# Kernel optimization log

Hardware: AMD Instinct MI355X
Metric: run time of the kernel (lower is better)

Reference implementation:

```python
import jax, jax.numpy as jnp
import numpy as np

NUM_HEADS = 16
INACTIVE = 4          # cfg_comp.attention_heads_inactive
SIG_DIM = 64          # cfg_comp.attention_heads_signature_dim
MLP_HIDDEN = 512      # cfg_comp.attention_heads_inference_mlp_hidden


def setup_inputs() -> dict:
    key = jax.random.key(0)
    ks = jax.random.split(key, 16)
    S, B, E = 2048, 2, 1024
    def xavier(k, shape, gain=1.0):
        fan_in, fan_out = shape[1], shape[0]
        a = gain * np.sqrt(6.0 / (fan_in + fan_out))
        return jax.random.uniform(k, shape, jnp.float32, -a, a)
    g = 1.0 / np.sqrt(2.0)
    return {
        "query": jax.random.normal(ks[0], (S, B, E), jnp.float32),
        "q_w": xavier(ks[1], (E, E), g), "q_b": jnp.zeros((E,), jnp.float32),
        "k_w": xavier(ks[2], (E, E), g), "k_b": jnp.zeros((E,), jnp.float32),
        "v_w": xavier(ks[3], (E, E), g), "v_b": jnp.zeros((E,), jnp.float32),
        "out_w": xavier(ks[4], (E, E)), "out_b": jnp.zeros((E,), jnp.float32),
        "inf1_w": xavier(ks[5], (MLP_HIDDEN, E), np.sqrt(2.0)),
        "inf1_b": jnp.zeros((MLP_HIDDEN,), jnp.float32),
        "inf2_w": xavier(ks[6], (SIG_DIM, MLP_HIDDEN), np.sqrt(2.0)),
        "inf2_b": jnp.zeros((SIG_DIM,), jnp.float32),
        "head_sig": jax.random.normal(ks[7], (NUM_HEADS, SIG_DIM), jnp.float32)
                    * np.sqrt(2.0 / (NUM_HEADS + SIG_DIM)),
    }


def _head_mask(query, inf1_w, inf1_b, inf2_w, inf2_b, head_sig):
    # inference_masking_step: (S, B, E) -> binary mask (B, H, S)
    t = jax.nn.relu(query @ inf1_w.T + inf1_b)          # (S, B, hidden)
    t = t @ inf2_w.T + inf2_b                            # (S, B, sig)
    s = t @ head_sig.T                                   # (S, B, H) head scores
    keep = NUM_HEADS - INACTIVE
    kth = jax.lax.top_k(s, keep)[0][..., -1]             # (S, B) kth-largest score
    mask = (s >= kth[..., None]).astype(query.dtype)     # 1 at top-`keep` heads
    mask = jax.lax.stop_gradient(mask)                   # scatter of constants in torch
    return jnp.transpose(mask, (1, 2, 0))                # (B, H, S)


def reference(query, q_w, q_b, k_w, k_b, v_w, v_b, out_w, out_b,
              inf1_w, inf1_b, inf2_w, inf2_b, head_sig):
    S, B, E = query.shape
    H, D = NUM_HEADS, E // NUM_HEADS
    scaling = D ** (-0.5)

    q = (query @ q_w.T + q_b) * scaling                  # (S, B, E)
    k = query @ k_w.T + k_b
    v = query @ v_w.T + v_b
    # (S, B, E) -> (B, H, S, D)
    to_bhsd = lambda x: jnp.transpose(x.reshape(S, B, H, D), (1, 2, 0, 3))
    q, k, v = to_bhsd(q), to_bhsd(k), to_bhsd(v)

    attn = jax.nn.softmax(jnp.einsum("bhqd,bhkd->bhqk", q, k), axis=-1)
    o = jnp.einsum("bhqk,bhkd->bhqd", attn, v)           # (B, H, S, D)

    mask = _head_mask(query, inf1_w, inf1_b, inf2_w, inf2_b, head_sig)  # (B, H, S)
    o = o * mask[..., None]                              # gate per head per position

    out = jnp.transpose(o, (2, 0, 1, 3)).reshape(S, B, E)
    return out @ out_w.T + out_b
```

## Files before the change

kernel.cpp:

```cpp
#include <hip/hip_runtime.h>
#include <hip/hip_bf16.h>

#define S_LEN 2048
#define BATCH 2
#define EDIM 1024
#define NHEAD 16
#define DHEAD 64
#define HIDDEN 512
#define SIGD 64
#define KEEP 12

typedef __attribute__((ext_vector_type(8))) short bf16x8;
typedef __attribute__((ext_vector_type(4))) float f32x4;

static __device__ __forceinline__ float bf2f(short s) {
  unsigned int u = ((unsigned int)(unsigned short)s) << 16;
  float f; __builtin_memcpy(&f, &u, 4); return f;
}
static __device__ __forceinline__ short f2bf(float f) {
  unsigned int u; __builtin_memcpy(&u, &f, 4);
  u += 0x7fffu + ((u >> 16) & 1u);
  return (short)(u >> 16);
}

#if __has_builtin(__builtin_amdgcn_exp2f)
static __device__ __forceinline__ float fexp2(float x) { return __builtin_amdgcn_exp2f(x); }
#else
static __device__ __forceinline__ float fexp2(float x) { return exp2f(x); }
#endif

static __device__ __forceinline__ void gl_lds16(const short* g, short* l) {
  __builtin_amdgcn_global_load_lds(
      (const __attribute__((address_space(1))) unsigned int*)g,
      (__attribute__((address_space(3))) unsigned int*)l, 16, 0, 0);
}

template<int CTRL>
static __device__ __forceinline__ float dpp_movf(float x) {
  return __builtin_bit_cast(float, __builtin_amdgcn_update_dpp(
      0, __builtin_bit_cast(int, x), CTRL, 0xF, 0xF, true));
}
static __device__ __forceinline__ float row_max16(float v) {
  v = fmaxf(v, dpp_movf<0x128>(v));
  v = fmaxf(v, dpp_movf<0x124>(v));
  v = fmaxf(v, dpp_movf<0x122>(v));
  v = fmaxf(v, dpp_movf<0x121>(v));
  return v;
}
static __device__ __forceinline__ float row_sum16(float v) {
  v += dpp_movf<0x128>(v);
  v += dpp_movf<0x124>(v);
  v += dpp_movf<0x122>(v);
  v += dpp_movf<0x121>(v);
  return v;
}

__global__ __launch_bounds__(256) void cvt_all(
    const float* __restrict__ query, const float* __restrict__ inf1_w,
    const float* __restrict__ qw, const float* __restrict__ kw,
    const float* __restrict__ vw, const float* __restrict__ ow,
    short* __restrict__ qh, short* __restrict__ ql,
    short* __restrict__ w1h, short* __restrict__ w1l,
    short* __restrict__ Wq, short* __restrict__ Wk,
    short* __restrict__ Wv, short* __restrict__ Wo)
{
  int blk = blockIdx.x;
  if (blk < 4608) {
    const float* in; short *oh, *ol; int i;
    if (blk < 4096) { in = query;  oh = qh;  ol = ql;  i = (blk * 256 + threadIdx.x) * 4; }
    else            { in = inf1_w; oh = w1h; ol = w1l; i = ((blk - 4096) * 256 + threadIdx.x) * 4; }
    float4 f = *(const float4*)(in + i);
    union { short s[4]; uint2 v; } uh, ul;
    float x[4] = {f.x, f.y, f.z, f.w};
    #pragma unroll
    for (int u = 0; u < 4; ++u) {
      short h = f2bf(x[u]);
      uh.s[u] = h;
      ul.s[u] = f2bf(x[u] - bf2f(h));
    }
    *(uint2*)(oh + i) = uh.v;
    *(uint2*)(ol + i) = ul.v;
  } else {
    int t = blk - 4608;
    int mat = t >> 10, sub = t & 1023;
    const float* in = (mat == 0) ? qw : (mat == 1) ? kw : (mat == 2) ? vw : ow;
    short* out      = (mat == 0) ? Wq : (mat == 1) ? Wk : (mat == 2) ? Wv : Wo;
    int i = (sub * 256 + threadIdx.x) * 4;
    float4 f = *(const float4*)(in + i);
    union { short s[4]; uint2 v; } u;
    u.s[0] = f2bf(f.x); u.s[1] = f2bf(f.y); u.s[2] = f2bf(f.z); u.s[3] = f2bf(f.w);
    *(uint2*)(out + i) = u.v;
  }
}

template<bool F32OUT>
static __device__ __forceinline__ void gemm128_body(
    short* smem,
    const short* __restrict__ A, const short* __restrict__ B,
    const float* __restrict__ bias, void* __restrict__ outv,
    int row0, int col0, float scale)
{
  short* As = smem;
  short* Bs = smem + 128*32;
  const int tid  = threadIdx.x;
  const int wave = tid >> 6, lane = tid & 63;
  const int quad = lane >> 4, l16 = lane & 15;
  const int wr = wave >> 1, wc = wave & 1;
  const int lr = lane >> 2, lc8 = (lane & 3) * 8;

  const short* gA = A + (size_t)(row0 + wave*16 + lr) * EDIM + lc8;
  const short* gB = B + (size_t)(col0 + wave*16 + lr) * EDIM + lc8;
  short* lA = As + wave*512;
  short* lB = Bs + wave*512;

  f32x4 acc[4][4] = {};
  gl_lds16(gA, lA);  gl_lds16(gA + 64*EDIM, lA + 64*32);
  gl_lds16(gB, lB);  gl_lds16(gB + 64*EDIM, lB + 64*32);

  for (int k0 = 0; k0 < EDIM; k0 += 32) {
    __syncthreads();
    bf16x8 af[4], bfr[4];
    #pragma unroll
    for (int i = 0; i < 4; ++i)
      af[i] = *(const bf16x8*)&As[(wr*64 + i*16 + l16)*32 + quad*8];
    #pragma unroll
    for (int j = 0; j < 4; ++j)
      bfr[j] = *(const bf16x8*)&Bs[(wc*64 + j*16 + l16)*32 + quad*8];
    __syncthreads();
    if (k0 + 32 < EDIM) {
      const short* gA2 = gA + k0 + 32;
      const short* gB2 = gB + k0 + 32;
      gl_lds16(gA2, lA);  gl_lds16(gA2 + 64*EDIM, lA + 64*32);
      gl_lds16(gB2, lB);  gl_lds16(gB2 + 64*EDIM, lB + 64*32);
    }
    #pragma unroll
    for (int i = 0; i < 4; ++i)
      #pragma unroll
      for (int j = 0; j < 4; ++j)
        acc[i][j] = __builtin_amdgcn_mfma_f32_16x16x32_bf16(af[i], bfr[j], acc[i][j], 0, 0, 0);
  }
  #pragma unroll
  for (int j = 0; j < 4; ++j) {
    int col = col0 + wc*64 + j*16 + l16;
    float bv = bias[col];
    #pragma unroll
    for (int i = 0; i < 4; ++i) {
      int rowb = row0 + wr*64 + i*16 + quad*4;
      #pragma unroll
      for (int r = 0; r < 4; ++r) {
        float v = (acc[i][j][r] + bv) * scale;
        if constexpr (F32OUT) {
          ((float*)outv)[(size_t)(rowb + r) * EDIM + col] = v;
        } else {
          ((short*)outv)[(size_t)(rowb + r) * EDIM + col] = f2bf(v);
        }
      }
    }
  }
}

static __device__ __forceinline__ void gemm_t1_body(
    short* smem,
    const short* __restrict__ Agh, const short* __restrict__ Agl,
    const short* __restrict__ Bgh, const short* __restrict__ Bgl,
    const float* __restrict__ bias, float* __restrict__ T1,
    int row0, int col0)
{
  short* Ah = smem;
  short* Al = smem + 4096;
  short* Bh = smem + 8192;
  short* Bl = smem + 10240;
  const int tid  = threadIdx.x;
  const int wave = tid >> 6, lane = tid & 63;
  const int quad = lane >> 4, l16 = lane & 15;
  const int wr = wave >> 1, wc = wave & 1;
  const int lr = lane >> 2, lc8 = (lane & 3) * 8;

  const short* gAh = Agh + (size_t)(row0 + wave*16 + lr) * EDIM + lc8;
  const short* gAl = Agl + (size_t)(row0 + wave*16 + lr) * EDIM + lc8;
  const short* gBh = Bgh + (size_t)(col0 + wave*16 + lr) * EDIM + lc8;
  const short* gBl = Bgl + (size_t)(col0 + wave*16 + lr) * EDIM + lc8;
  short* lAh = Ah + wave*512;  short* lAl = Al + wave*512;
  short* lBh = Bh + wave*512;  short* lBl = Bl + wave*512;

  f32x4 acc[4][2] = {};
  gl_lds16(gAh, lAh);  gl_lds16(gAh + 64*EDIM, lAh + 64*32);
  gl_lds16(gAl, lAl);  gl_lds16(gAl + 64*EDIM, lAl + 64*32);
  gl_lds16(gBh, lBh);  gl_lds16(gBl, lBl);

  for (int k0 = 0; k0 < EDIM; k0 += 32) {
    __syncthreads();
    bf16x8 ah[4], al[4], bh[2], bl[2];
    #pragma unroll
    for (int i = 0; i < 4; ++i) {
      ah[i] = *(const bf16x8*)&Ah[(wr*64 + i*16 + l16)*32 + quad*8];
      al[i] = *(const bf16x8*)&Al[(wr*64 + i*16 + l16)*32 + quad*8];
    }
    #pragma unroll
    for (int j = 0; j < 2; ++j) {
      bh[j] = *(const bf16x8*)&Bh[(wc*32 + j*16 + l16)*32 + quad*8];
      bl[j] = *(const bf16x8*)&Bl[(wc*32 + j*16 + l16)*32 + quad*8];
    }
    __syncthreads();
    if (k0 + 32 < EDIM) {
      const short* p;
      p = gAh + k0 + 32;  gl_lds16(p, lAh);  gl_lds16(p + 64*EDIM, lAh + 64*32);
      p = gAl + k0 + 32;  gl_lds16(p, lAl);  gl_lds16(p + 64*EDIM, lAl + 64*32);
      gl_lds16(gBh + k0 + 32, lBh);  gl_lds16(gBl + k0 + 32, lBl);
    }
    #pragma unroll
    for (int i = 0; i < 4; ++i)
      #pragma unroll
      for (int j = 0; j < 2; ++j) {
        acc[i][j] = __builtin_amdgcn_mfma_f32_16x16x32_bf16(ah[i], bh[j], acc[i][j], 0, 0, 0);
        acc[i][j] = __builtin_amdgcn_mfma_f32_16x16x32_bf16(ah[i], bl[j], acc[i][j], 0, 0, 0);
        acc[i][j] = __builtin_amdgcn_mfma_f32_16x16x32_bf16(al[i], bh[j], acc[i][j], 0, 0, 0);
      }
  }
  #pragma unroll
  for (int j = 0; j < 2; ++j) {
    int col = col0 + wc*32 + j*16 + l16;
    float bv = bias[col];
    #pragma unroll
    for (int i = 0; i < 4; ++i) {
      int rowb = row0 + wr*64 + i*16 + quad*4;
      #pragma unroll
      for (int r = 0; r < 4; ++r)
        T1[(size_t)(rowb + r) * HIDDEN + col] = fmaxf(acc[i][j][r] + bv, 0.0f);
    }
  }
}

__global__ __launch_bounds__(256) void mega_gemm1(
    const short* __restrict__ qh, const short* __restrict__ ql,
    const short* __restrict__ w1h, const short* __restrict__ w1l,
    const float* __restrict__ inf1_b, float* __restrict__ T1,
    const short* __restrict__ Wq, const short* __restrict__ Wk,
    const short* __restrict__ Wv,
    const float* __restrict__ qb, const float* __restrict__ kb,
    const float* __restrict__ vb,
    short* __restrict__ Qp, short* __restrict__ Kp, short* __restrict__ Vp)
{
  __shared__ __attribute__((aligned(16))) short smem[12288];
  int blk = blockIdx.x;
  if ((blk & 3) == 3) {
    int id = blk >> 2;
    gemm_t1_body(smem, qh, ql, w1h, w1l, inf1_b, T1,
                 (id & 31) * 128, (id >> 5) * 64);
  } else {
    int id = (blk >> 2) * 3 + (blk & 3);
    int row0 = (id & 31) * 128;
    int rest = id >> 5;
    int mat = rest >> 3, cb = rest & 7;
    const short* B   = (mat == 0) ? Wq : (mat == 1) ? Wk : Wv;
    const float* bia = (mat == 0) ? qb : (mat == 1) ? kb : vb;
    short* out       = (mat == 0) ? Qp : (mat == 1) ? Kp : Vp;
    float scale      = (mat == 0) ? 0.18033688011112042f : 1.0f;
    gemm128_body<false>(smem, qh, B, bia, (void*)out, row0, cb * 128, scale);
  }
}

__global__ __launch_bounds__(256) void mid_kernel(
    const float* __restrict__ T1, const float* __restrict__ inf2_w,
    const float* __restrict__ inf2_b, const float* __restrict__ head_sig,
    float* __restrict__ maskbuf,
    const short* __restrict__ Vp, short* __restrict__ VT)
{
  __shared__ __attribute__((aligned(16))) float fsm[16*HIDDEN + 16*SIGD + 16*NHEAD];
  int blk = blockIdx.x;
  const int tid = threadIdx.x;
  if (blk < 256) {
    float (*t1s)[HIDDEN] = (float(*)[HIDDEN])fsm;
    float (*t2s)[SIGD]   = (float(*)[SIGD])(fsm + 16*HIDDEN);
    float (*ss)[NHEAD]   = (float(*)[NHEAD])(fsm + 16*HIDDEN + 16*SIGD);
    const int tok0 = blk * 16;
    {
      int row = tid >> 4, c0 = (tid & 15) * 32;
      const float* src = T1 + (size_t)(tok0 + row) * HIDDEN + c0;
      #pragma unroll
      for (int u = 0; u < 8; ++u)
        *(float4*)&t1s[row][c0 + u*4] = *(const float4*)(src + u*4);
    }
    __syncthreads();
    #pragma unroll
    for (int it = 0; it < 4; ++it) {
      int idx = tid + it * 256;
      int tok = idx >> 6, j = idx & 63;
      const float4* w4 = (const float4*)(inf2_w + (size_t)j * HIDDEN);
      const float4* t4 = (const float4*)(&t1s[tok][0]);
      float a = inf2_b[j];
      for (int k = 0; k < HIDDEN/4; ++k) {
        float4 wv = w4[k], tv = t4[k];
        a += tv.x*wv.x + tv.y*wv.y + tv.z*wv.z + tv.w*wv.w;
      }
      t2s[tok][j] = a;
    }
    __syncthreads();
    {
      int tok = tid >> 4, h = tid & 15;
      float a = 0.f;
      for (int d = 0; d < SIGD; ++d) a += t2s[tok][d] * head_sig[h*SIGD + d];
      ss[tok][h] = a;
    }
    __syncthreads();
    {
      int tok = tid >> 4, h = tid & 15;
      float sv = ss[tok][h];
      int cnt = 0;
      #pragma unroll
      for (int j = 0; j < NHEAD; ++j) cnt += (ss[tok][j] > sv) ? 1 : 0;
      int gt = tok0 + tok;
      int s = gt >> 1, b = gt & 1;
      maskbuf[((size_t)(b*NHEAD + h)) * S_LEN + s] = (cnt < KEEP) ? 1.0f : 0.0f;
    }
  } else {
    short (*tile)[72] = (short(*)[72])fsm;
    int t = blk - 256;
    const int s0 = (t & 31) * 64, e0 = ((t >> 5) & 15) * 64, b = t >> 9;
    {
      int sr = tid >> 2, ec = (tid & 3) * 16;
      const short* src = Vp + (size_t)(s0 + sr) * 2048 + b * 1024 + e0 + ec;
      *(uint4*)&tile[sr][ec]     = *(const uint4*)src;
      *(uint4*)&tile[sr][ec + 8] = *(const uint4*)(src + 8);
    }
    __syncthreads();
    {
      int er = tid >> 2, sc = (tid & 3) * 16;
      unsigned pack[8];
      #pragma unroll
      for (int u = 0; u < 8; ++u) {
        unsigned lo = (unsigned short)tile[sc + 2*u][er];
        unsigned hi = (unsigned short)tile[sc + 2*u + 1][er];
        pack[u] = lo | (hi << 16);
      }
      short* dst = VT + (size_t)(b * 1024 + e0 + er) * 2048 + s0 + sc;
      *(uint4*)(dst)     = *(uint4*)&pack[0];
      *(uint4*)(dst + 8) = *(uint4*)&pack[4];
    }
  }
}

__global__ __launch_bounds__(256) void flash_attn(
    short* QpOg, const short* __restrict__ Kp, const short* __restrict__ VT,
    const float* __restrict__ maskbuf)
{
  __shared__ __attribute__((aligned(16))) short Ks[64][68];
  __shared__ __attribute__((aligned(16))) short Vt[64][68];
  __shared__ __attribute__((aligned(16))) short uni[4352];
  const int bh = blockIdx.x;
  const int b = bh >> 4, h = bh & 15;
  const int q0 = blockIdx.y * 64;
  const int tid = threadIdx.x;
  const int wave = tid >> 6, lane = tid & 63;
  const int quad = lane >> 4, l16 = lane & 15;
  const size_t colbase = (size_t)b * EDIM + h * DHEAD;
  const size_t rstride = (size_t)BATCH * EDIM;

  const int r4 = tid >> 2, c16 = (tid & 3) * 16;
  const short* gK = Kp + (size_t)r4 * rstride + colbase + c16;
  const short* gV = VT + (size_t)(bh * 64 + r4) * S_LEN + c16;

  {
    const short* src = QpOg + (size_t)(q0 + r4) * rstride + colbase + c16;
    *(uint4*)&uni[r4*68 + c16]     = *(const uint4*)src;
    *(uint4*)&uni[r4*68 + c16 + 8] = *(const uint4*)(src + 8);
  }
  __syncthreads();
  bf16x8 aq0 = *(const bf16x8*)&uni[(wave*16 + l16)*68 + quad*8];
  bf16x8 aq1 = *(const bf16x8*)&uni[(wave*16 + l16)*68 + 32 + quad*8];
  short* Psw = &uni[wave * 1088];

  uint4 kr0 = *(const uint4*)(gK);      uint4 kr1 = *(const uint4*)(gK + 8);
  uint4 vr0 = *(const uint4*)(gV);      uint4 vr1 = *(const uint4*)(gV + 8);

  float m_i[4], l_i[4];
  f32x4 oacc[4];
  #pragma unroll
  for (int r = 0; r < 4; ++r) { m_i[r] = -1e30f; l_i[r] = 0.f; }
  #pragma unroll
  for (int dt = 0; dt < 4; ++dt) oacc[dt] = f32x4{0.f, 0.f, 0.f, 0.f};

  for (int kv0 = 0; kv0 < S_LEN; kv0 += 64) {
    __syncthreads();
    *(uint4*)&Ks[r4][c16]     = kr0;
    *(uint4*)&Ks[r4][c16 + 8] = kr1;
    *(uint4*)&Vt[r4][c16]     = vr0;
    *(uint4*)&Vt[r4][c16 + 8] = vr1;
    __syncthreads();
    if (kv0 + 64 < S_LEN) {
      const short* nK = gK + (size_t)(kv0 + 64) * rstride;
      const short* nV = gV + (kv0 + 64);
      kr0 = *(const uint4*)nK;  kr1 = *(const uint4*)(nK + 8);
      vr0 = *(const uint4*)nV;  vr1 = *(const uint4*)(nV + 8);
    }
    f32x4 sacc[4];
    #pragma unroll
    for (int c = 0; c < 4; ++c) sacc[c] = f32x4{0.f, 0.f, 0.f, 0.f};
    __builtin_amdgcn_s_setprio(1);
    #pragma unroll
    for (int c = 0; c < 4; ++c) {
      bf16x8 b0 = *(const bf16x8*)&Ks[c*16 + l16][quad*8];
      bf16x8 b1 = *(const bf16x8*)&Ks[c*16 + l16][32 + quad*8];
      sacc[c] = __builtin_amdgcn_mfma_f32_16x16x32_bf16(aq0, b0, sacc[c], 0, 0, 0);
      sacc[c] = __builtin_amdgcn_mfma_f32_16x16x32_bf16(aq1, b1, sacc[c], 0, 0, 0);
    }
    __builtin_amdgcn_s_setprio(0);
    #pragma unroll
    for (int r = 0; r < 4; ++r) {
      float vmax = fmaxf(fmaxf(sacc[0][r], sacc[1][r]),
                         fmaxf(sacc[2][r], sacc[3][r]));
      vmax = row_max16(vmax);
      float mnew = fmaxf(m_i[r], vmax);
      float alpha = fexp2(m_i[r] - mnew);
      float rsum = 0.f;
      short* prow = &Psw[(quad*4 + r)*68 + l16];
      #pragma unroll
      for (int p = 0; p < 2; ++p) {
        float ea = fexp2(sacc[2*p][r]   - mnew);
        float eb = fexp2(sacc[2*p+1][r] - mnew);
        unsigned pk = __builtin_amdgcn_perm(
            __builtin_bit_cast(unsigned, eb),
            __builtin_bit_cast(unsigned, ea), 0x07060302u);
        prow[(2*p)*16]     = (short)(pk & 0xffffu);
        prow[(2*p + 1)*16] = (short)(pk >> 16);
        rsum += ea + eb;
      }
      rsum = row_sum16(rsum);
      l_i[r] = l_i[r] * alpha + rsum;
      m_i[r] = mnew;
      #pragma unroll
      for (int dt = 0; dt < 4; ++dt) oacc[dt][r] *= alpha;
    }
    asm volatile("s_waitcnt lgkmcnt(0)" ::: "memory");
    __builtin_amdgcn_s_setprio(1);
    #pragma unroll
    for (int ks = 0; ks < 2; ++ks) {
      bf16x8 ap = *(const bf16x8*)&Psw[l16*68 + ks*32 + quad*8];
      #pragma unroll
      for (int dt = 0; dt < 4; ++dt) {
        bf16x8 bb = *(const bf16x8*)&Vt[dt*16 + l16][ks*32 + quad*8];
        oacc[dt] = __builtin_amdgcn_mfma_f32_16x16x32_bf16(ap, bb, oacc[dt], 0, 0, 0);
      }
    }
    __builtin_amdgcn_s_setprio(0);
  }
  #pragma unroll
  for (int r = 0; r < 4; ++r) {
    int s = q0 + wave*16 + quad*4 + r;
    float mk = maskbuf[((size_t)(b*NHEAD + h)) * S_LEN + s];
    float scale = mk / l_i[r];
    short* dst = QpOg + (size_t)s * rstride + colbase;
    #pragma unroll
    for (int dt = 0; dt < 4; ++dt)
      dst[dt*16 + l16] = f2bf(oacc[dt][r] * scale);
  }
}

__global__ __launch_bounds__(256) void gemm_out(
    const short* __restrict__ A, const short* __restrict__ W,
    const float* __restrict__ bias, float* __restrict__ out)
{
  __shared__ __attribute__((aligned(16))) short smem[8192];
  gemm128_body<true>(smem, A, W, bias, (void*)out,
                     blockIdx.x * 128, blockIdx.y * 128, 1.0f);
}

extern "C" void kernel_launch(void* const* d_in, const int* in_sizes, int n_in,
                              void* d_out, int out_size, void* d_ws, size_t ws_size,
                              hipStream_t stream)
{
  const float* query   = (const float*)d_in[0];
  const float* q_w     = (const float*)d_in[1];
  const float* q_b     = (const float*)d_in[2];
  const float* k_w     = (const float*)d_in[3];
  const float* k_b     = (const float*)d_in[4];
  const float* v_w     = (const float*)d_in[5];
  const float* v_b     = (const float*)d_in[6];
  const float* out_w   = (const float*)d_in[7];
  const float* out_b   = (const float*)d_in[8];
  const float* inf1_w  = (const float*)d_in[9];
  const float* inf1_b  = (const float*)d_in[10];
  const float* inf2_w  = (const float*)d_in[11];
  const float* inf2_b  = (const float*)d_in[12];
  const float* head_sig= (const float*)d_in[13];

  char* ws = (char*)d_ws;
  short* qh      = (short*)(ws);
  short* VTb     = (short*)(ws);
  short* ql      = (short*)(ws + (size_t)( 8u<<20));
  float* maskbuf = (float*)(ws + (size_t)( 8u<<20));
  short* Qp      = (short*)(ws + (size_t)(16u<<20));
  short* Kp      = (short*)(ws + (size_t)(24u<<20));
  short* Vp      = (short*)(ws + (size_t)(32u<<20));
  short* Wo      = (short*)(ws + (size_t)(40u<<20));
  char* ob = (char*)d_out;
  float* T1  = (float*)(ob);
  short* w1h = (short*)(ob + (size_t)( 8u<<20));
  short* w1l = (short*)(ob + (size_t)( 9u<<20));
  short* Wq  = (short*)(ob + (size_t)(10u<<20));
  short* Wk  = (short*)(ob + (size_t)(12u<<20));
  short* Wv  = (short*)(ob + (size_t)(14u<<20));
  float* out = (float*)d_out;

  dim3 blk(256);
  cvt_all<<<dim3(8704), blk, 0, stream>>>(query, inf1_w, q_w, k_w, v_w, out_w,
                                          qh, ql, w1h, w1l, Wq, Wk, Wv, Wo);
  mega_gemm1<<<dim3(1024), blk, 0, stream>>>(qh, ql, w1h, w1l, inf1_b, T1,
                                             Wq, Wk, Wv, q_b, k_b, v_b, Qp, Kp, Vp);
  mid_kernel<<<dim3(1280), blk, 0, stream>>>(T1, inf2_w, inf2_b, head_sig, maskbuf,
                                             Vp, VTb);
  flash_attn<<<dim3(32, 32), blk, 0, stream>>>(Qp, Kp, VTb, maskbuf);
  gemm_out<<<dim3(32, 8), blk, 0, stream>>>(Qp, Wo, out_b, out);
}
```

Before: 353.8 us.

## Double KV tile to 128 and skip rescale when max grows little

Measured after the change: 361.0 us. 2.0% more time.

```diff
diff --git a/kernel.cpp b/kernel.cpp
--- a/kernel.cpp
+++ b/kernel.cpp
@@ -344,9 +344,9 @@
     short* QpOg, const short* __restrict__ Kp, const short* __restrict__ VT,
     const float* __restrict__ maskbuf)
 {
-  __shared__ __attribute__((aligned(16))) short Ks[64][68];
-  __shared__ __attribute__((aligned(16))) short Vt[64][68];
-  __shared__ __attribute__((aligned(16))) short uni[4352];
+  __shared__ __attribute__((aligned(16))) short Ks[128][68];
+  __shared__ __attribute__((aligned(16))) short Vt[2][64][68];
+  __shared__ __attribute__((aligned(16))) short uni[8704];
   const int bh = blockIdx.x;
   const int b = bh >> 4, h = bh & 15;
   const int q0 = blockIdx.y * 64;
@@ -368,10 +368,16 @@
   __syncthreads();
   bf16x8 aq0 = *(const bf16x8*)&uni[(wave*16 + l16)*68 + quad*8];
   bf16x8 aq1 = *(const bf16x8*)&uni[(wave*16 + l16)*68 + 32 + quad*8];
-  short* Psw = &uni[wave * 1088];
-
-  uint4 kr0 = *(const uint4*)(gK);      uint4 kr1 = *(const uint4*)(gK + 8);
-  uint4 vr0 = *(const uint4*)(gV);      uint4 vr1 = *(const uint4*)(gV + 8);
+  short* Psw = &uni[wave * 2176];
+
+  uint4 ka0 = *(const uint4*)(gK);
+  uint4 ka1 = *(const uint4*)(gK + 8);
+  uint4 kb0 = *(const uint4*)(gK + 64*rstride);
+  uint4 kb1 = *(const uint4*)(gK + 64*rstride + 8);
+  uint4 va0 = *(const uint4*)(gV);
+  uint4 va1 = *(const uint4*)(gV + 8);
+  uint4 vb0 = *(const uint4*)(gV + 64);
+  uint4 vb1 = *(const uint4*)(gV + 72);
 
   float m_i[4], l_i[4];
   f32x4 oacc[4];
@@ -380,25 +386,35 @@
   #pragma unroll
   for (int dt = 0; dt < 4; ++dt) oacc[dt] = f32x4{0.f, 0.f, 0.f, 0.f};
 
-  for (int kv0 = 0; kv0 < S_LEN; kv0 += 64) {
-    __syncthreads();
-    *(uint4*)&Ks[r4][c16]     = kr0;
-    *(uint4*)&Ks[r4][c16 + 8] = kr1;
-    *(uint4*)&Vt[r4][c16]     = vr0;
-    *(uint4*)&Vt[r4][c16 + 8] = vr1;
-    __syncthreads();
-    if (kv0 + 64 < S_LEN) {
-      const short* nK = gK + (size_t)(kv0 + 64) * rstride;
-      const short* nV = gV + (kv0 + 64);
-      kr0 = *(const uint4*)nK;  kr1 = *(const uint4*)(nK + 8);
-      vr0 = *(const uint4*)nV;  vr1 = *(const uint4*)(nV + 8);
-    }
-    f32x4 sacc[4];
-    #pragma unroll
-    for (int c = 0; c < 4; ++c) sacc[c] = f32x4{0.f, 0.f, 0.f, 0.f};
+  for (int kv0 = 0; kv0 < S_LEN; kv0 += 128) {
+    __syncthreads();
+    *(uint4*)&Ks[r4][c16]        = ka0;
+    *(uint4*)&Ks[r4][c16 + 8]    = ka1;
+    *(uint4*)&Ks[r4+64][c16]     = kb0;
+    *(uint4*)&Ks[r4+64][c16 + 8] = kb1;
+    *(uint4*)&Vt[0][r4][c16]     = va0;
+    *(uint4*)&Vt[0][r4][c16 + 8] = va1;
+    *(uint4*)&Vt[1][r4][c16]     = vb0;
+    *(uint4*)&Vt[1][r4][c16 + 8] = vb1;
+    __syncthreads();
+    if (kv0 + 128 < S_LEN) {
+      const short* nK = gK + (size_t)(kv0 + 128) * rstride;
+      const short* nV = gV + (kv0 + 128);
+      ka0 = *(const uint4*)nK;
+      ka1 = *(const uint4*)(nK + 8);
+      kb0 = *(const uint4*)(nK + 64*rstride);
+      kb1 = *(const uint4*)(nK + 64*rstride + 8);
+      va0 = *(const uint4*)nV;
+      va1 = *(const uint4*)(nV + 8);
+      vb0 = *(const uint4*)(nV + 64);
+      vb1 = *(const uint4*)(nV + 72);
+    }
+    f32x4 sacc[8];
+    #pragma unroll
+    for (int c = 0; c < 8; ++c) sacc[c] = f32x4{0.f, 0.f, 0.f, 0.f};
     __builtin_amdgcn_s_setprio(1);
     #pragma unroll
-    for (int c = 0; c < 4; ++c) {
+    for (int c = 0; c < 8; ++c) {
       bf16x8 b0 = *(const bf16x8*)&Ks[c*16 + l16][quad*8];
       bf16x8 b1 = *(const bf16x8*)&Ks[c*16 + l16][32 + quad*8];
       sacc[c] = __builtin_amdgcn_mfma_f32_16x16x32_bf16(aq0, b0, sacc[c], 0, 0, 0);
@@ -407,38 +423,44 @@
     __builtin_amdgcn_s_setprio(0);
     #pragma unroll
     for (int r = 0; r < 4; ++r) {
-      float vmax = fmaxf(fmaxf(sacc[0][r], sacc[1][r]),
-                         fmaxf(sacc[2][r], sacc[3][r]));
+      float vmax = fmaxf(fmaxf(fmaxf(sacc[0][r], sacc[1][r]),
+                               fmaxf(sacc[2][r], sacc[3][r])),
+                         fmaxf(fmaxf(sacc[4][r], sacc[5][r]),
+                               fmaxf(sacc[6][r], sacc[7][r])));
       vmax = row_max16(vmax);
-      float mnew = fmaxf(m_i[r], vmax);
-      float alpha = fexp2(m_i[r] - mnew);
+      if (!__all(vmax <= m_i[r] + 8.0f)) {
+        float mnew = fmaxf(m_i[r], vmax);
+        float alpha = fexp2(m_i[r] - mnew);
+        l_i[r] *= alpha;
+        #pragma unroll
+        for (int dt = 0; dt < 4; ++dt) oacc[dt][r] *= alpha;
+        m_i[r] = mnew;
+      }
       float rsum = 0.f;
       short* prow = &Psw[(quad*4 + r)*68 + l16];
       #pragma unroll
-      for (int p = 0; p < 2; ++p) {
-        float ea = fexp2(sacc[2*p][r]   - mnew);
-        float eb = fexp2(sacc[2*p+1][r] - mnew);
+      for (int p = 0; p < 4; ++p) {
+        float ea = fexp2(sacc[2*p][r]   - m_i[r]);
+        float eb = fexp2(sacc[2*p+1][r] - m_i[r]);
         unsigned pk = __builtin_amdgcn_perm(
             __builtin_bit_cast(unsigned, eb),
             __builtin_bit_cast(unsigned, ea), 0x07060302u);
-        prow[(2*p)*16]     = (short)(pk & 0xffffu);
-        prow[(2*p + 1)*16] = (short)(pk >> 16);
+        short* pr = prow + (p >> 1) * 1088;
+        pr[(2*(p & 1))*16]     = (short)(pk & 0xffffu);
+        pr[(2*(p & 1) + 1)*16] = (short)(pk >> 16);
         rsum += ea + eb;
       }
       rsum = row_sum16(rsum);
-      l_i[r] = l_i[r] * alpha + rsum;
-      m_i[r] = mnew;
-      #pragma unroll
-      for (int dt = 0; dt < 4; ++dt) oacc[dt][r] *= alpha;
+      l_i[r] += rsum;
     }
     asm volatile("s_waitcnt lgkmcnt(0)" ::: "memory");
     __builtin_amdgcn_s_setprio(1);
     #pragma unroll
-    for (int ks = 0; ks < 2; ++ks) {
-      bf16x8 ap = *(const bf16x8*)&Psw[l16*68 + ks*32 + quad*8];
+    for (int ks = 0; ks < 4; ++ks) {
+      bf16x8 ap = *(const bf16x8*)&Psw[(ks>>1)*1088 + l16*68 + (ks&1)*32 + quad*8];
       #pragma unroll
       for (int dt = 0; dt < 4; ++dt) {
-        bf16x8 bb = *(const bf16x8*)&Vt[dt*16 + l16][ks*32 + quad*8];
+        bf16x8 bb = *(const bf16x8*)&Vt[ks>>1][dt*16 + l16][(ks&1)*32 + quad*8];
         oacc[dt] = __builtin_amdgcn_mfma_f32_16x16x32_bf16(ap, bb, oacc[dt], 0, 0, 0);
       }
     }
```
